# Performance work log

Hardware: AMD Instinct MI355X
Metric: run time of the kernel (lower is better)

Reference implementation:

```python
import jax, jax.numpy as jnp
import numpy as np

NUM_QUBITS = 8
QD = 2 ** NUM_QUBITS          # 256
PI = float(np.pi)
D_MODEL = 512
NUM_HEADS = 8
HEAD_DIM = D_MODEL // NUM_HEADS
LN_EPS = 1e-5


def _superposition(feat):
    # torch bug faithfully reproduced: state starts as e0 and is *multiplied*
    # by per-qubit amplitudes, so only index 0 survives. All values real.
    B, S, d = feat.shape
    idx = np.arange(NUM_QUBITS) % d
    theta = feat[:, :, idx] * PI                       # [B,S,nq]
    cos_h = jnp.cos(theta * 0.5)
    sin_h = jnp.sin(theta * 0.5)
    mask = (np.arange(QD)[None, :] >> np.arange(NUM_QUBITS)[:, None]) & 1  # [nq,QD]
    amps = jnp.where(mask[None, None] == 0, cos_h[..., None], sin_h[..., None])  # [B,S,nq,QD]
    prod = jnp.prod(amps, axis=2)                      # [B,S,QD]
    e0 = jnp.zeros((QD,), feat.dtype).at[0].set(1.0)
    state = prod * e0
    norm = jnp.sqrt(jnp.sum(state * state, axis=-1, keepdims=True))
    return state / (norm + 1e-10)


def _linear_entangle(ent):
    # entangle_matrix is block-diagonal with symmetric 2x2 blocks [[a,a],[a,-a]];
    # state @ M.T == pairwise 2x2 matmul (identical math, avoids 65536^2 matrix)
    B, S, D = ent.shape
    a = 0.7071
    M = jnp.array([[a, a], [a, -a]], ent.dtype)
    return (ent.reshape(B, S, D // 2, 2) @ M).reshape(B, S, D)


def _layer_norm(x, g, b):
    m = jnp.mean(x, axis=-1, keepdims=True)
    v = jnp.mean((x - m) ** 2, axis=-1, keepdims=True)
    return (x - m) * jax.lax.rsqrt(v + LN_EPS) * g + b


def setup_inputs() -> dict:
    key = jax.random.key(0)
    ks = jax.random.split(key, 16)
    D = D_MODEL
    s = 1.0 / np.sqrt(D)
    inp = {
        'audio_features': jax.random.normal(ks[0], (2, 256, D), jnp.float32),
        'visual_features': jax.random.normal(ks[1], (2, 256, D), jnp.float32),
        'Wq': jax.random.normal(ks[2], (D, D), jnp.float32) * s,
        'bq': jnp.zeros((D,), jnp.float32),
        'Wk': jax.random.normal(ks[3], (D, D), jnp.float32) * s,
        'bk': jnp.zeros((D,), jnp.float32),
        'Wv': jax.random.normal(ks[4], (D, D), jnp.float32) * s,
        'bv': jnp.zeros((D,), jnp.float32),
        'Wo': jax.random.normal(ks[5], (D, D), jnp.float32) * s,
        'bo': jnp.zeros((D,), jnp.float32),
        'We': jax.random.normal(ks[6], (D, D), jnp.float32) * s,
        'be': jnp.zeros((D,), jnp.float32),
        'gamma': jnp.ones((D,), jnp.float32),
        'beta': jnp.zeros((D,), jnp.float32),
    }
    return inp


def reference(audio_features, visual_features, Wq, bq, Wk, bk, Wv, bv,
              Wo, bo, We, be, gamma, beta):
    B, S, D = audio_features.shape
    H, hd = NUM_HEADS, HEAD_DIM

    aq = audio_features @ Wq + bq
    av = audio_features @ Wv + bv
    vk = visual_features @ Wk + bk
    vv = visual_features @ Wv + bv

    qa = _superposition(audio_features @ We + be)    # [B,S,QD]
    qv = _superposition(visual_features @ We + be)   # [B,S,QD]
    ent = (qa[..., :, None] * qv[..., None, :]).reshape(B, S, QD * QD)
    ent = _linear_entangle(ent)                      # [B,S,QD^2]

    probs = ent * ent
    qsum = jnp.sum(probs, axis=-1)                   # [B,S]
    ang = jnp.where(ent < 0, PI, 0.0)                # angle of a real number
    interference = jnp.cos(jnp.mean(ang, axis=-1))   # [B,S]
    scale = (qsum * interference)[:, None, :, None]  # [B,1,S,1]

    def heads(x):
        return x.reshape(B, S, H, hd).transpose(0, 2, 1, 3)

    aqh, vkh, vvh, avh = heads(aq), heads(vk), heads(vv), heads(av)
    logits = scale * jnp.einsum('bhqd,bhkd->bhqk', aqh, vkh) / np.sqrt(hd)
    attn = jax.nn.softmax(logits, axis=-1)           # [B,H,S,S]

    audio_att = jnp.einsum('bhqk,bhkd->bhqd', attn, vvh)
    visual_att = jnp.einsum('bhqk,bhqd->bhkd', attn, avh)
    audio_out = audio_att.transpose(0, 2, 1, 3).reshape(B, S, D) @ Wo + bo
    visual_out = visual_att.transpose(0, 2, 1, 3).reshape(B, S, D) @ Wo + bo

    audio_final = _layer_norm(audio_features + audio_out, gamma, beta)
    visual_final = _layer_norm(visual_features + visual_out, gamma, beta)

    quantum_coherence = jnp.mean(jnp.abs(ent))
    pn = probs / (jnp.sum(probs, axis=-1, keepdims=True) + 1e-10)
    entanglement_entropy = jnp.mean(-jnp.sum(pn * jnp.log(pn + 1e-10), axis=-1))

    return (audio_final, visual_final, quantum_coherence,
            entanglement_entropy, attn[:, -1])
```

## Files before the change

kernel.cpp:

```cpp
#include <hip/hip_runtime.h>
#include <math.h>

#define PI_F 3.14159265358979323846f

typedef __attribute__((ext_vector_type(8))) short short8v;
typedef __attribute__((ext_vector_type(4))) float f32x4;
typedef __attribute__((ext_vector_type(16))) float f32x16;

__device__ __forceinline__ unsigned short f2bf(float f) {
    unsigned int u = __float_as_uint(f);
    u += 0x7fffu + ((u >> 16) & 1u);
    return (unsigned short)(u >> 16);
}

__device__ __forceinline__ unsigned int cvtpk_bf16(float lo, float hi) {
    unsigned int r;
    asm("v_cvt_pk_bf16_f32 %0, %1, %2" : "=v"(r) : "v"(lo), "v"(hi));
    return r;
}

union W8 { unsigned int w[4]; short8v v; };

__device__ __forceinline__ void gload_lds16(const void* g, void* l) {
    __builtin_amdgcn_global_load_lds((const __attribute__((address_space(1))) unsigned int*)g,
                                     (__attribute__((address_space(3))) unsigned int*)l, 16, 0, 0);
}

__global__ __launch_bounds__(256) void prep_tok(const float* __restrict__ audio,
                                                const float* __restrict__ visual,
                                                const float* __restrict__ Wq,
                                                const float* __restrict__ Wk,
                                                const float* __restrict__ Wv,
                                                const float* __restrict__ Wo,
                                                const float* __restrict__ We,
                                                const float* __restrict__ be,
                                                unsigned short* __restrict__ audio_b,
                                                unsigned short* __restrict__ visual_b,
                                                unsigned short* __restrict__ Wqt,
                                                unsigned short* __restrict__ Wkt,
                                                unsigned short* __restrict__ Wvt,
                                                unsigned short* __restrict__ Wot,
                                                float* __restrict__ scale,
                                                float* __restrict__ coh_tok,
                                                float* __restrict__ ent_tok) {
    __shared__ float tile[32][33];
    const int bid = blockIdx.x;
    if (bid < 1536) {
        const int z = bid >> 8;
        const int x0 = (bid & 15) * 32, y0 = ((bid >> 4) & 15) * 32;
        const int tx = threadIdx.x & 31, ty = threadIdx.x >> 5;
        if (z < 2) {
            const float* src = z ? visual : audio;
            unsigned short* dst = z ? visual_b : audio_b;
#pragma unroll
            for (int i = 0; i < 4; i++) {
                int r = y0 + ty + i * 8;
                dst[r * 512 + x0 + tx] = f2bf(src[r * 512 + x0 + tx]);
            }
        } else {
            const float* src = (z == 2) ? Wq : (z == 3) ? Wk : (z == 4) ? Wv : Wo;
            unsigned short* dst = (z == 2) ? Wqt : (z == 3) ? Wkt : (z == 4) ? Wvt : Wot;
#pragma unroll
            for (int i = 0; i < 4; i++)
                tile[ty + i * 8][tx] = src[(y0 + ty + i * 8) * 512 + x0 + tx];
            __syncthreads();
#pragma unroll
            for (int i = 0; i < 4; i++) {
                int n = x0 + ty + i * 8;
                dst[n * 512 + y0 + tx] = f2bf(tile[tx][ty + i * 8]);
            }
        }
    } else {
        const int t = (bid - 1536) * 4 + (threadIdx.x >> 6);
        const int lane = threadIdx.x & 63;
        float accA[8] = {}, accV[8] = {};
#pragma unroll
        for (int i = 0; i < 8; i++) {
            int k = i * 64 + lane;
            float wa = audio[t * 512 + k], wv = visual[t * 512 + k];
            const float* wrow = &We[k * 512];
#pragma unroll
            for (int c = 0; c < 8; c++) {
                float w = wrow[c];
                accA[c] += wa * w;
                accV[c] += wv * w;
            }
        }
#pragma unroll
        for (int c = 0; c < 8; c++) {
#pragma unroll
            for (int o = 32; o >= 1; o >>= 1) {
                accA[c] += __shfl_xor(accA[c], o);
                accV[c] += __shfl_xor(accV[c], o);
            }
        }
        if (lane == 0) {
            float pa = 1.f, pv = 1.f;
#pragma unroll
            for (int c = 0; c < 8; c++) {
                pa *= cosf((accA[c] + be[c]) * (PI_F * 0.5f));
                pv *= cosf((accV[c] + be[c]) * (PI_F * 0.5f));
            }
            float s0a = pa / (fabsf(pa) + 1e-10f);
            float s0v = pv / (fabsf(pv) + 1e-10f);
            float e = s0a * s0v;
            const float a = 0.7071f;
            float ent0 = a * e;
            float qsum = 2.f * ent0 * ent0;
            float interf = (ent0 < 0.f) ? cosf(2.f * PI_F / 65536.f) : 1.f;
            scale[t] = qsum * interf;
            coh_tok[t] = 2.f * fabsf(ent0);
            float p = (ent0 * ent0) / (qsum + 1e-10f);
            ent_tok[t] = -2.f * p * logf(p + 1e-10f);
        }
    }
}

struct MfmaArgs {
    const unsigned short* A[4];
    const unsigned short* Bt[4];
    const float* bias[4];
    void* C[4];
    int obf[4];
    int otr[4];
};

__global__ __launch_bounds__(256) void gemm_mfma(MfmaArgs args) {
    const int zb = blockIdx.z;
    const unsigned short* __restrict__ A = args.A[zb];
    const unsigned short* __restrict__ Bt = args.Bt[zb];
    const float* __restrict__ bias = args.bias[zb];
    const int otr = args.otr[zb];

    const int n0 = blockIdx.x * 32;
    const int m0 = blockIdx.y * 32;

    __shared__ unsigned short As[32 * 512];
    __shared__ unsigned short Bs[32 * 512];

    const int tid = threadIdx.x;
    const int lane = tid & 63;
    const int wid = tid >> 6;
    const int wr = wid >> 1, wc = wid & 1;
    const int l15 = lane & 15;
    const int lhi = lane >> 4;

#pragma unroll
    for (int i = 0; i < 8; i++) {
        int row = i * 4 + wid;
        int lc = lane ^ row;
        gload_lds16(A + (size_t)(m0 + row) * 512 + lc * 8,
                    (char*)As + row * 1024);
        gload_lds16(Bt + (size_t)(n0 + row) * 512 + lc * 8,
                    (char*)Bs + row * 1024);
    }
    __syncthreads();

    f32x4 acc = {};
    const int arow = wr * 16 + l15;
    const int brow = wc * 16 + l15;
#pragma unroll
    for (int ks = 0; ks < 16; ks++) {
        const int lcr = ks * 4 + lhi;
        short8v a = *(const short8v*)((const char*)As + arow * 1024 + ((lcr ^ arow) << 4));
        short8v b = *(const short8v*)((const char*)Bs + brow * 1024 + ((lcr ^ brow) << 4));
        if (otr)
            acc = __builtin_amdgcn_mfma_f32_16x16x32_bf16(b, a, acc, 0, 0, 0);
        else
            acc = __builtin_amdgcn_mfma_f32_16x16x32_bf16(a, b, acc, 0, 0, 0);
    }

    if (otr) {
        unsigned short* __restrict__ Ct = (unsigned short*)args.C[zb];
#pragma unroll
        for (int r = 0; r < 4; r++) {
            int nrow = n0 + wc * 16 + lhi * 4 + r;
            int tcol = m0 + wr * 16 + l15;
            Ct[nrow * 512 + tcol] = f2bf(acc[r] + bias[nrow]);
        }
    } else if (args.obf[zb]) {
        unsigned short* __restrict__ Cb = (unsigned short*)args.C[zb];
#pragma unroll
        for (int r = 0; r < 4; r++) {
            int row = m0 + wr * 16 + lhi * 4 + r;
            int col = n0 + wc * 16 + l15;
            Cb[row * 512 + col] = f2bf(acc[r] + bias[col]);
        }
    } else {
        float* __restrict__ C = (float*)args.C[zb];
#pragma unroll
        for (int r = 0; r < 4; r++) {
            int row = m0 + wr * 16 + lhi * 4 + r;
            int col = n0 + wc * 16 + l15;
            C[row * 512 + col] = acc[r] + bias[col];
        }
    }
}

__global__ __launch_bounds__(512, 2) void attn_roles(const unsigned short* __restrict__ aqb,
                                                     const unsigned short* __restrict__ vkb,
                                                     const unsigned short* __restrict__ vvt,
                                                     const unsigned short* __restrict__ avt,
                                                     const float* __restrict__ scale,
                                                     const float* __restrict__ coh,
                                                     const float* __restrict__ entt,
                                                     unsigned short* __restrict__ attcat_b,
                                                     float* __restrict__ attn_last,
                                                     float* __restrict__ scal_out) {
    __shared__ char smem[65536];
    char* Kb = smem;
    char* VF = smem + 32768;

    const int tid = threadIdx.x;
    const int wid = tid >> 6;
    const int lane = tid & 63;
    const int lq = lane & 31;
    const int hi = lane >> 5;

    if (blockIdx.x == 8) {
        if (blockIdx.y || blockIdx.z) return;
        float c = coh[tid], e = entt[tid];
#pragma unroll
        for (int o = 32; o >= 1; o >>= 1) {
            c += __shfl_xor(c, o);
            e += __shfl_xor(e, o);
        }
        float* rc = (float*)smem;
        float* re = rc + 8;
        if (lane == 0) { rc[wid] = c; re[wid] = e; }
        __syncthreads();
        if (tid == 0) {
            float cs = 0.f, es = 0.f;
#pragma unroll
            for (int i = 0; i < 8; i++) { cs += rc[i]; es += re[i]; }
            scal_out[0] = cs / (512.f * 65536.f);
            scal_out[1] = es / 512.f;
        }
        return;
    }

    const int h = blockIdx.x, b = blockIdx.y, role = blockIdx.z;

    short8v qf[4];
    {
        const unsigned short* qbase = aqb + (size_t)(b * 256 + wid * 32 + lq) * 512 + h * 64;
#pragma unroll
        for (int s = 0; s < 4; s++) qf[s] = *(const short8v*)(qbase + (2 * s + hi) * 8);
    }
    const float sq = scale[b * 256 + wid * 32 + lq] * 0.125f;

    {
#pragma unroll
        for (int i = 0; i < 4; i++) {
            int r = wid * 32 + i * 8 + (lane >> 3);
            int lc = (lane & 7) ^ (r & 7);
            gload_lds16(vkb + (size_t)(b * 256 + r) * 512 + h * 64 + lc * 8,
                        Kb + wid * 4096 + i * 1024);
        }
    }

    {
        const unsigned short* tsrc = (role == 0) ? vvt : avt;
#pragma unroll
        for (int i = 0; i < 4; i++) {
            gload_lds16(tsrc + (size_t)(h * 64 + 32 * hi + lq) * 512 + b * 256 + 32 * wid + 8 * i,
                        VF + wid * 4096 + i * 1024);
        }
    }
    __syncthreads();

    f32x16 p[8] = {};
#pragma unroll
    for (int t = 0; t < 8; t++) {
        const int krow = t * 32 + lq;
#pragma unroll
        for (int s = 0; s < 4; s++) {
            int slot = (2 * s + hi) ^ (krow & 7);
            short8v kf = *(const short8v*)(Kb + krow * 128 + (slot << 4));
            p[t] = __builtin_amdgcn_mfma_f32_32x32x16_bf16(kf, qf[s], p[t], 0, 0, 0);
        }
    }

    {
        float mx = -1e30f;
#pragma unroll
        for (int t = 0; t < 8; t++) {
            p[t] *= sq;
#pragma unroll
            for (int r = 0; r < 16; r++) mx = fmaxf(mx, p[t][r]);
        }
        mx = fmaxf(mx, __shfl_xor(mx, 32));
        float sum = 0.f;
#pragma unroll
        for (int t = 0; t < 8; t++)
#pragma unroll
            for (int r = 0; r < 16; r++) {
                float e = __expf(p[t][r] - mx);
                p[t][r] = e;
                sum += e;
            }
        sum += __shfl_xor(sum, 32);
        float inv = 1.0f / sum;
#pragma unroll
        for (int t = 0; t < 8; t++) p[t] *= inv;
    }

    if (role == 0) {
        f32x16 aacc[2] = {};
#pragma unroll
        for (int t = 0; t < 8; t++) {
            unsigned int c0 = cvtpk_bf16(p[t][0], p[t][1]);
            unsigned int c1 = cvtpk_bf16(p[t][2], p[t][3]);
            unsigned int c2 = cvtpk_bf16(p[t][4], p[t][5]);
            unsigned int c3 = cvtpk_bf16(p[t][6], p[t][7]);
            unsigned int e0 = (unsigned int)__shfl_xor((int)c0, 32);
            unsigned int e1 = (unsigned int)__shfl_xor((int)c1, 32);
            unsigned int e2 = (unsigned int)__shfl_xor((int)c2, 32);
            unsigned int e3 = (unsigned int)__shfl_xor((int)c3, 32);
            W8 fa0;
            fa0.w[0] = hi ? e2 : c0;
            fa0.w[1] = hi ? e3 : c1;
            fa0.w[2] = hi ? c2 : e0;
            fa0.w[3] = hi ? c3 : e1;
            unsigned int c4 = cvtpk_bf16(p[t][8], p[t][9]);
            unsigned int c5 = cvtpk_bf16(p[t][10], p[t][11]);
            unsigned int c6 = cvtpk_bf16(p[t][12], p[t][13]);
            unsigned int c7 = cvtpk_bf16(p[t][14], p[t][15]);
            unsigned int e4 = (unsigned int)__shfl_xor((int)c4, 32);
            unsigned int e5 = (unsigned int)__shfl_xor((int)c5, 32);
            unsigned int e6 = (unsigned int)__shfl_xor((int)c6, 32);
            unsigned int e7 = (unsigned int)__shfl_xor((int)c7, 32);
            W8 fa1;
            fa1.w[0] = hi ? e6 : c4;
            fa1.w[1] = hi ? e7 : c5;
            fa1.w[2] = hi ? c6 : e4;
            fa1.w[3] = hi ? c7 : e5;
#pragma unroll
            for (int dt = 0; dt < 2; dt++) {
                short8v vf = *(const short8v*)(VF + ((((t * 4 + hi) * 2 + dt) * 32 + lq) << 4));
                aacc[dt] = __builtin_amdgcn_mfma_f32_32x32x16_bf16(fa0.v, vf, aacc[dt], 0, 0, 0);
                short8v vg = *(const short8v*)(VF + ((((t * 4 + hi + 2) * 2 + dt) * 32 + lq) << 4));
                aacc[dt] = __builtin_amdgcn_mfma_f32_32x32x16_bf16(fa1.v, vg, aacc[dt], 0, 0, 0);
            }
        }
#pragma unroll
        for (int dt = 0; dt < 2; dt++)
#pragma unroll
            for (int r = 0; r < 16; r++) {
                int qrow = wid * 32 + (r & 3) + 8 * (r >> 2) + 4 * hi;
                attcat_b[(size_t)(b * 256 + qrow) * 512 + h * 64 + 32 * dt + lq] = f2bf(aacc[dt][r]);
            }
        __syncthreads();

        if (h == 7) {
            float* tile = (float*)smem + (size_t)wid * (32 * 33);
            const int q2 = lane >> 1, koff = (lane & 1) * 16;
#pragma unroll
            for (int t = 0; t < 8; t++) {
#pragma unroll
                for (int r = 0; r < 16; r++)
                    tile[lq * 33 + ((r & 3) + 8 * (r >> 2) + 4 * hi)] = p[t][r];
                float* orow = attn_last + (size_t)(b * 256 + wid * 32 + q2) * 256 + 32 * t + koff;
#pragma unroll
                for (int j = 0; j < 16; j++) orow[j] = tile[q2 * 33 + koff + j];
            }
        }
        return;
    }

    __syncthreads();

    if ((wid >> 1) == 0) {
        const int dq = (wid & 1) * 32 + lq;
#pragma unroll
        for (int t = 0; t < 8; t++)
#pragma unroll
            for (int r = 0; r < 16; r++) {
                int k = 32 * t + (r & 3) + 8 * (r >> 2) + 4 * hi;
                int slot = (dq >> 3) ^ ((k ^ (k >> 3)) & 7);
                *(unsigned short*)(Kb + k * 128 + slot * 16 + (dq & 7) * 2) = f2bf(p[t][r]);
            }
    }
    __syncthreads();

    f32x16 vacc[2] = {};
    {
        const int krow = wid * 32 + lq;
        const int xr = (krow ^ (krow >> 3)) & 7;
#pragma unroll
        for (int c = 0; c < 4; c++) {
#pragma unroll
            for (int uc = 0; uc < 4; uc++) {
                int slot = (2 * uc + hi) ^ xr;
                short8v pa = *(const short8v*)(Kb + krow * 128 + slot * 16);
                int m = 2 * (4 * c + uc) + hi;
#pragma unroll
                for (int dt = 0; dt < 2; dt++) {
                    short8v af = *(const short8v*)(VF + (((m * 2 + dt) * 32 + lq) << 4));
                    vacc[dt] = __builtin_amdgcn_mfma_f32_32x32x16_bf16(pa, af, vacc[dt], 0, 0, 0);
                }
            }
            if (c < 3) {
                __syncthreads();
                if ((wid >> 1) == c + 1) {
                    const int dq = (wid & 1) * 32 + lq;
#pragma unroll
                    for (int t = 0; t < 8; t++)
#pragma unroll
                        for (int r = 0; r < 16; r++) {
                            int k = 32 * t + (r & 3) + 8 * (r >> 2) + 4 * hi;
                            int slot = (dq >> 3) ^ ((k ^ (k >> 3)) & 7);
                            *(unsigned short*)(Kb + k * 128 + slot * 16 + (dq & 7) * 2) = f2bf(p[t][r]);
                        }
                }
                __syncthreads();
            }
        }
    }
#pragma unroll
    for (int dt = 0; dt < 2; dt++)
#pragma unroll
        for (int r = 0; r < 16; r++) {
            int krow = wid * 32 + (r & 3) + 8 * (r >> 2) + 4 * hi;
            attcat_b[(size_t)(512 + b * 256 + krow) * 512 + h * 64 + 32 * dt + lq] = f2bf(vacc[dt][r]);
        }
}

__global__ __launch_bounds__(256) void ln_final(const float* __restrict__ xa,
                                                const float* __restrict__ xv,
                                                const float* __restrict__ proj,
                                                const float* __restrict__ gamma,
                                                const float* __restrict__ beta,
                                                float* __restrict__ out) {
    __shared__ float red[4];
    const int t = blockIdx.x;
    const int tid = threadIdx.x;
    const int wid = tid >> 6, lane = tid & 63;

    const float* x = (t < 512) ? (xa + t * 512) : (xv + (t - 512) * 512);
    const float* pp = proj + t * 512;

    float y0 = x[tid] + pp[tid];
    float y1 = x[tid + 256] + pp[tid + 256];

    float s = y0 + y1;
#pragma unroll
    for (int o = 32; o >= 1; o >>= 1) s += __shfl_xor(s, o);
    if (lane == 0) red[wid] = s;
    __syncthreads();
    float mean = (red[0] + red[1] + red[2] + red[3]) * (1.f / 512.f);

    float d0 = y0 - mean, d1 = y1 - mean;
    float v = d0 * d0 + d1 * d1;
    __syncthreads();
#pragma unroll
    for (int o = 32; o >= 1; o >>= 1) v += __shfl_xor(v, o);
    if (lane == 0) red[wid] = v;
    __syncthreads();
    float var = (red[0] + red[1] + red[2] + red[3]) * (1.f / 512.f);
    float rstd = rsqrtf(var + 1e-5f);

    out[t * 512 + tid] = d0 * rstd * gamma[tid] + beta[tid];
    out[t * 512 + tid + 256] = d1 * rstd * gamma[tid + 256] + beta[tid + 256];
}

extern "C" void kernel_launch(void* const* d_in, const int* in_sizes, int n_in,
                              void* d_out, int out_size, void* d_ws, size_t ws_size,
                              hipStream_t stream) {
    const float* audio  = (const float*)d_in[0];
    const float* visual = (const float*)d_in[1];
    const float* Wq = (const float*)d_in[2];
    const float* bq = (const float*)d_in[3];
    const float* Wk = (const float*)d_in[4];
    const float* bk = (const float*)d_in[5];
    const float* Wv = (const float*)d_in[6];
    const float* bv = (const float*)d_in[7];
    const float* Wo = (const float*)d_in[8];
    const float* bo = (const float*)d_in[9];
    const float* We = (const float*)d_in[10];
    const float* be = (const float*)d_in[11];
    const float* gamma = (const float*)d_in[12];
    const float* beta  = (const float*)d_in[13];
    float* out = (float*)d_out;

    float* ws = (float*)d_ws;
    float* proj  = ws;
    float* scale = ws + 524288;
    float* coh   = ws + 524800;
    float* entt  = ws + 525312;
    unsigned short* attcat_b = (unsigned short*)(ws + 525824);
    unsigned short* audio_b  = (unsigned short*)(ws + 787968);
    unsigned short* visual_b = (unsigned short*)(ws + 919040);
    unsigned short* Wqt  = (unsigned short*)(ws + 1050112);
    unsigned short* Wkt  = (unsigned short*)(ws + 1181184);
    unsigned short* Wvt  = (unsigned short*)(ws + 1312256);
    unsigned short* Wot  = (unsigned short*)(ws + 1443328);
    unsigned short* aq_b = (unsigned short*)(ws + 1574400);
    unsigned short* vk_b = (unsigned short*)(ws + 1705472);
    unsigned short* vvt  = (unsigned short*)(ws + 1836544);
    unsigned short* avt  = (unsigned short*)(ws + 1967616);

    hipLaunchKernelGGL(prep_tok, dim3(1664), dim3(256), 0, stream,
                       audio, visual, Wq, Wk, Wv, Wo, We, be,
                       audio_b, visual_b, Wqt, Wkt, Wvt, Wot,
                       scale, coh, entt);

    MfmaArgs g1;
    g1.A[0] = audio_b;  g1.Bt[0] = Wqt; g1.bias[0] = bq; g1.C[0] = aq_b; g1.obf[0] = 1; g1.otr[0] = 0;
    g1.A[1] = visual_b; g1.Bt[1] = Wkt; g1.bias[1] = bk; g1.C[1] = vk_b; g1.obf[1] = 1; g1.otr[1] = 0;
    g1.A[2] = visual_b; g1.Bt[2] = Wvt; g1.bias[2] = bv; g1.C[2] = vvt;  g1.obf[2] = 1; g1.otr[2] = 1;
    g1.A[3] = audio_b;  g1.Bt[3] = Wvt; g1.bias[3] = bv; g1.C[3] = avt;  g1.obf[3] = 1; g1.otr[3] = 1;
    hipLaunchKernelGGL(gemm_mfma, dim3(16, 16, 4), dim3(256), 0, stream, g1);

    hipLaunchKernelGGL(attn_roles, dim3(9, 2, 2), dim3(512), 0, stream,
                       aq_b, vk_b, vvt, avt, scale, coh, entt,
                       attcat_b, out + 524290, out + 524288);

    MfmaArgs g2;
    for (int i = 0; i < 4; i++) {
        g2.A[i] = attcat_b; g2.Bt[i] = Wot; g2.bias[i] = bo; g2.C[i] = proj;
        g2.obf[i] = 0; g2.otr[i] = 0;
    }
    hipLaunchKernelGGL(gemm_mfma, dim3(16, 32, 1), dim3(256), 0, stream, g2);

    hipLaunchKernelGGL(ln_final, dim3(1024), dim3(256), 0, stream,
                       audio, visual, proj, gamma, beta, out);
}
```

Before: 47.56 us.

## Fuse fp32-to-bf16 conversion and weight transpose into GEMM tile staging

Removes the separate prep kernel that converted activations to bf16 and transposed the weights into bf16 buffers. The projection GEMM and the output GEMM now read fp32 inputs and weights directly, converting and transposing them while staging tiles into shared memory, and the token-scale computation rides along in the same launch. This drops one kernel launch and the round trip through intermediate bf16 buffers. In exchange, each GEMM block redoes the conversion and does strided column loads of the weights, and each weight tile is converted many times across blocks.

```diff
diff --git a/kernel.cpp b/kernel.cpp
--- a/kernel.cpp
+++ b/kernel.cpp
@@ -26,53 +26,94 @@
                                      (__attribute__((address_space(3))) unsigned int*)l, 16, 0, 0);
 }
 
-__global__ __launch_bounds__(256) void prep_tok(const float* __restrict__ audio,
-                                                const float* __restrict__ visual,
-                                                const float* __restrict__ Wq,
-                                                const float* __restrict__ Wk,
-                                                const float* __restrict__ Wv,
-                                                const float* __restrict__ Wo,
-                                                const float* __restrict__ We,
-                                                const float* __restrict__ be,
-                                                unsigned short* __restrict__ audio_b,
-                                                unsigned short* __restrict__ visual_b,
-                                                unsigned short* __restrict__ Wqt,
-                                                unsigned short* __restrict__ Wkt,
-                                                unsigned short* __restrict__ Wvt,
-                                                unsigned short* __restrict__ Wot,
-                                                float* __restrict__ scale,
-                                                float* __restrict__ coh_tok,
-                                                float* __restrict__ ent_tok) {
-    __shared__ float tile[32][33];
+
+__device__ __forceinline__ void stageA_f32(const float* __restrict__ Af, int m0,
+                                           char* As, int tid) {
+    const int row = tid >> 3;
+    const int cb = tid & 7;
+#pragma unroll
+    for (int j = 0; j < 8; j++) {
+        int lc = cb + j * 8;
+        const float* p = Af + (size_t)(m0 + row) * 512 + lc * 8;
+        float4 a0 = *(const float4*)(p);
+        float4 a1 = *(const float4*)(p + 4);
+        W8 u;
+        u.w[0] = cvtpk_bf16(a0.x, a0.y);
+        u.w[1] = cvtpk_bf16(a0.z, a0.w);
+        u.w[2] = cvtpk_bf16(a1.x, a1.y);
+        u.w[3] = cvtpk_bf16(a1.z, a1.w);
+        *(short8v*)(As + row * 1024 + (((lc ^ row) & 63) << 4)) = u.v;
+    }
+}
+
+__device__ __forceinline__ void stageA_bf16(const unsigned short* __restrict__ Ab, int m0,
+                                            char* As, int lane, int wid) {
+#pragma unroll
+    for (int i = 0; i < 8; i++) {
+        int row = i * 4 + wid;
+        int lc = lane ^ row;
+        gload_lds16(Ab + (size_t)(m0 + row) * 512 + lc * 8, As + row * 1024);
+    }
+}
+
+__device__ __forceinline__ void stageB_tr(const float* __restrict__ W, int n0,
+                                          char* Bs, int tid) {
+    const int n = tid & 31;
+    const int kbase = (tid >> 5) * 2;
+#pragma unroll
+    for (int i = 0; i < 32; i++) {
+        int k = kbase + i * 16;
+        float lo = W[(size_t)k * 512 + n0 + n];
+        float hi = W[(size_t)(k + 1) * 512 + n0 + n];
+        unsigned int pk = cvtpk_bf16(lo, hi);
+        *(unsigned int*)(Bs + n * 1024 + (((k >> 3) ^ n) & 63) * 16 + (k & 7) * 2) = pk;
+    }
+}
+
+__device__ __forceinline__ f32x4 gemm_core(const char* As, const char* Bs,
+                                           int wr, int wc, int l15, int lhi, int otr) {
+    f32x4 acc = {};
+    const int arow = wr * 16 + l15;
+    const int brow = wc * 16 + l15;
+#pragma unroll
+    for (int ks = 0; ks < 16; ks++) {
+        const int lcr = ks * 4 + lhi;
+        short8v a = *(const short8v*)(As + arow * 1024 + ((lcr ^ arow) << 4));
+        short8v b = *(const short8v*)(Bs + brow * 1024 + ((lcr ^ brow) << 4));
+        if (otr)
+            acc = __builtin_amdgcn_mfma_f32_16x16x32_bf16(b, a, acc, 0, 0, 0);
+        else
+            acc = __builtin_amdgcn_mfma_f32_16x16x32_bf16(a, b, acc, 0, 0, 0);
+    }
+    return acc;
+}
+
+__global__ __launch_bounds__(256) void gemm1_fused(const float* __restrict__ audio,
+                                                   const float* __restrict__ visual,
+                                                   const float* __restrict__ Wq,
+                                                   const float* __restrict__ Wk,
+                                                   const float* __restrict__ Wv,
+                                                   const float* __restrict__ We,
+                                                   const float* __restrict__ be,
+                                                   const float* __restrict__ bq,
+                                                   const float* __restrict__ bk,
+                                                   const float* __restrict__ bv,
+                                                   unsigned short* __restrict__ aq_b,
+                                                   unsigned short* __restrict__ vk_b,
+                                                   unsigned short* __restrict__ vvt,
+                                                   unsigned short* __restrict__ avt,
+                                                   float* __restrict__ scale,
+                                                   float* __restrict__ coh_tok,
+                                                   float* __restrict__ ent_tok) {
+    __shared__ char As[32 * 1024];
+    __shared__ char Bs[32 * 1024];
+
     const int bid = blockIdx.x;
-    if (bid < 1536) {
-        const int z = bid >> 8;
-        const int x0 = (bid & 15) * 32, y0 = ((bid >> 4) & 15) * 32;
-        const int tx = threadIdx.x & 31, ty = threadIdx.x >> 5;
-        if (z < 2) {
-            const float* src = z ? visual : audio;
-            unsigned short* dst = z ? visual_b : audio_b;
-#pragma unroll
-            for (int i = 0; i < 4; i++) {
-                int r = y0 + ty + i * 8;
-                dst[r * 512 + x0 + tx] = f2bf(src[r * 512 + x0 + tx]);
-            }
-        } else {
-            const float* src = (z == 2) ? Wq : (z == 3) ? Wk : (z == 4) ? Wv : Wo;
-            unsigned short* dst = (z == 2) ? Wqt : (z == 3) ? Wkt : (z == 4) ? Wvt : Wot;
-#pragma unroll
-            for (int i = 0; i < 4; i++)
-                tile[ty + i * 8][tx] = src[(y0 + ty + i * 8) * 512 + x0 + tx];
-            __syncthreads();
-#pragma unroll
-            for (int i = 0; i < 4; i++) {
-                int n = x0 + ty + i * 8;
-                dst[n * 512 + y0 + tx] = f2bf(tile[tx][ty + i * 8]);
-            }
-        }
-    } else {
-        const int t = (bid - 1536) * 4 + (threadIdx.x >> 6);
-        const int lane = threadIdx.x & 63;
+    const int tid = threadIdx.x;
+
+    if (bid >= 1024) {
+        const int t = (bid - 1024) * 4 + (tid >> 6);
+        const int lane = tid & 63;
         float accA[8] = {}, accV[8] = {};
 #pragma unroll
         for (int i = 0; i < 8; i++) {
@@ -113,31 +154,59 @@
             float p = (ent0 * ent0) / (qsum + 1e-10f);
             ent_tok[t] = -2.f * p * logf(p + 1e-10f);
         }
-    }
-}
-
-struct MfmaArgs {
-    const unsigned short* A[4];
-    const unsigned short* Bt[4];
-    const float* bias[4];
-    void* C[4];
-    int obf[4];
-    int otr[4];
-};
-
-__global__ __launch_bounds__(256) void gemm_mfma(MfmaArgs args) {
-    const int zb = blockIdx.z;
-    const unsigned short* __restrict__ A = args.A[zb];
-    const unsigned short* __restrict__ Bt = args.Bt[zb];
-    const float* __restrict__ bias = args.bias[zb];
-    const int otr = args.otr[zb];
+        return;
+    }
+
+    const int z = bid >> 8;
+    const int rem = bid & 255;
+    const int n0 = (rem & 15) * 32;
+    const int m0 = (rem >> 4) * 32;
+
+    const float* A = (z == 0 || z == 3) ? audio : visual;
+    const float* W = (z == 0) ? Wq : (z == 1) ? Wk : Wv;
+    const float* bias = (z == 0) ? bq : (z == 1) ? bk : bv;
+    const int otr = (z >= 2);
+
+    stageA_f32(A, m0, As, tid);
+    stageB_tr(W, n0, Bs, tid);
+    __syncthreads();
+
+    const int lane = tid & 63;
+    const int wid = tid >> 6;
+    const int wr = wid >> 1, wc = wid & 1;
+    const int l15 = lane & 15;
+    const int lhi = lane >> 4;
+
+    f32x4 acc = gemm_core(As, Bs, wr, wc, l15, lhi, otr);
+
+    if (otr) {
+        unsigned short* Ct = (z == 2) ? vvt : avt;
+#pragma unroll
+        for (int r = 0; r < 4; r++) {
+            int nrow = n0 + wc * 16 + lhi * 4 + r;
+            int tcol = m0 + wr * 16 + l15;
+            Ct[(size_t)nrow * 512 + tcol] = f2bf(acc[r] + bias[nrow]);
+        }
+    } else {
+        unsigned short* Cb = (z == 0) ? aq_b : vk_b;
+#pragma unroll
+        for (int r = 0; r < 4; r++) {
+            int row = m0 + wr * 16 + lhi * 4 + r;
+            int col = n0 + wc * 16 + l15;
+            Cb[(size_t)row * 512 + col] = f2bf(acc[r] + bias[col]);
+        }
+    }
+}
+
+__global__ __launch_bounds__(256) void gemm2_k(const unsigned short* __restrict__ Ab,
+                                               const float* __restrict__ Wo,
+                                               const float* __restrict__ bo,
+                                               float* __restrict__ C) {
+    __shared__ char As[32 * 1024];
+    __shared__ char Bs[32 * 1024];
 
     const int n0 = blockIdx.x * 32;
     const int m0 = blockIdx.y * 32;
-
-    __shared__ unsigned short As[32 * 512];
-    __shared__ unsigned short Bs[32 * 512];
-
     const int tid = threadIdx.x;
     const int lane = tid & 63;
     const int wid = tid >> 6;
@@ -145,55 +214,17 @@
     const int l15 = lane & 15;
     const int lhi = lane >> 4;
 
-#pragma unroll
-    for (int i = 0; i < 8; i++) {
-        int row = i * 4 + wid;
-        int lc = lane ^ row;
-        gload_lds16(A + (size_t)(m0 + row) * 512 + lc * 8,
-                    (char*)As + row * 1024);
-        gload_lds16(Bt + (size_t)(n0 + row) * 512 + lc * 8,
-                    (char*)Bs + row * 1024);
-    }
-    __syncthreads();
-
-    f32x4 acc = {};
-    const int arow = wr * 16 + l15;
-    const int brow = wc * 16 + l15;
-#pragma unroll
-    for (int ks = 0; ks < 16; ks++) {
-        const int lcr = ks * 4 + lhi;
-        short8v a = *(const short8v*)((const char*)As + arow * 1024 + ((lcr ^ arow) << 4));
-        short8v b = *(const short8v*)((const char*)Bs + brow * 1024 + ((lcr ^ brow) << 4));
-        if (otr)
-            acc = __builtin_amdgcn_mfma_f32_16x16x32_bf16(b, a, acc, 0, 0, 0);
-        else
-            acc = __builtin_amdgcn_mfma_f32_16x16x32_bf16(a, b, acc, 0, 0, 0);
-    }
-
-    if (otr) {
-        unsigned short* __restrict__ Ct = (unsigned short*)args.C[zb];
-#pragma unroll
-        for (int r = 0; r < 4; r++) {
-            int nrow = n0 + wc * 16 + lhi * 4 + r;
-            int tcol = m0 + wr * 16 + l15;
-            Ct[nrow * 512 + tcol] = f2bf(acc[r] + bias[nrow]);
-        }
-    } else if (args.obf[zb]) {
-        unsigned short* __restrict__ Cb = (unsigned short*)args.C[zb];
-#pragma unroll
-        for (int r = 0; r < 4; r++) {
-            int row = m0 + wr * 16 + lhi * 4 + r;
-            int col = n0 + wc * 16 + l15;
-            Cb[row * 512 + col] = f2bf(acc[r] + bias[col]);
-        }
-    } else {
-        float* __restrict__ C = (float*)args.C[zb];
-#pragma unroll
-        for (int r = 0; r < 4; r++) {
-            int row = m0 + wr * 16 + lhi * 4 + r;
-            int col = n0 + wc * 16 + l15;
-            C[row * 512 + col] = acc[r] + bias[col];
-        }
+    stageA_bf16(Ab, m0, As, lane, wid);
+    stageB_tr(Wo, n0, Bs, tid);
+    __syncthreads();
+
+    f32x4 acc = gemm_core(As, Bs, wr, wc, l15, lhi, 0);
+
+#pragma unroll
+    for (int r = 0; r < 4; r++) {
+        int row = m0 + wr * 16 + lhi * 4 + r;
+        int col = n0 + wc * 16 + l15;
+        C[(size_t)row * 512 + col] = acc[r] + bo[col];
     }
 }
 
@@ -489,39 +520,21 @@
     float* coh   = ws + 524800;
     float* entt  = ws + 525312;
     unsigned short* attcat_b = (unsigned short*)(ws + 525824);
-    unsigned short* audio_b  = (unsigned short*)(ws + 787968);
-    unsigned short* visual_b = (unsigned short*)(ws + 919040);
-    unsigned short* Wqt  = (unsigned short*)(ws + 1050112);
-    unsigned short* Wkt  = (unsigned short*)(ws + 1181184);
-    unsigned short* Wvt  = (unsigned short*)(ws + 1312256);
-    unsigned short* Wot  = (unsigned short*)(ws + 1443328);
-    unsigned short* aq_b = (unsigned short*)(ws + 1574400);
-    unsigned short* vk_b = (unsigned short*)(ws + 1705472);
-    unsigned short* vvt  = (unsigned short*)(ws + 1836544);
-    unsigned short* avt  = (unsigned short*)(ws + 1967616);
-
-    hipLaunchKernelGGL(prep_tok, dim3(1664), dim3(256), 0, stream,
-                       audio, visual, Wq, Wk, Wv, Wo, We, be,
-                       audio_b, visual_b, Wqt, Wkt, Wvt, Wot,
-                       scale, coh, entt);
-
-    MfmaArgs g1;
-    g1.A[0] = audio_b;  g1.Bt[0] = Wqt; g1.bias[0] = bq; g1.C[0] = aq_b; g1.obf[0] = 1; g1.otr[0] = 0;
-    g1.A[1] = visual_b; g1.Bt[1] = Wkt; g1.bias[1] = bk; g1.C[1] = vk_b; g1.obf[1] = 1; g1.otr[1] = 0;
-    g1.A[2] = visual_b; g1.Bt[2] = Wvt; g1.bias[2] = bv; g1.C[2] = vvt;  g1.obf[2] = 1; g1.otr[2] = 1;
-    g1.A[3] = audio_b;  g1.Bt[3] = Wvt; g1.bias[3] = bv; g1.C[3] = avt;  g1.obf[3] = 1; g1.otr[3] = 1;
-    hipLaunchKernelGGL(gemm_mfma, dim3(16, 16, 4), dim3(256), 0, stream, g1);
+    unsigned short* aq_b = (unsigned short*)(ws + 787968);
+    unsigned short* vk_b = (unsigned short*)(ws + 919040);
+    unsigned short* vvt  = (unsigned short*)(ws + 1050112);
+    unsigned short* avt  = (unsigned short*)(ws + 1181184);
+
+    hipLaunchKernelGGL(gemm1_fused, dim3(1152), dim3(256), 0, stream,
+                       audio, visual, Wq, Wk, Wv, We, be, bq, bk, bv,
+                       aq_b, vk_b, vvt, avt, scale, coh, entt);
 
     hipLaunchKernelGGL(attn_roles, dim3(9, 2, 2), dim3(512), 0, stream,
                        aq_b, vk_b, vvt, avt, scale, coh, entt,
                        attcat_b, out + 524290, out + 524288);
 
-    MfmaArgs g2;
-    for (int i = 0; i < 4; i++) {
-        g2.A[i] = attcat_b; g2.Bt[i] = Wot; g2.bias[i] = bo; g2.C[i] = proj;
-        g2.obf[i] = 0; g2.otr[i] = 0;
-    }
-    hipLaunchKernelGGL(gemm_mfma, dim3(16, 32, 1), dim3(256), 0, stream, g2);
+    hipLaunchKernelGGL(gemm2_k, dim3(16, 32), dim3(256), 0, stream,
+                       attcat_b, Wo, bo, proj);
 
     hipLaunchKernelGGL(ln_final, dim3(1024), dim3(256), 0, stream,
                        audio, visual, proj, gamma, beta, out);
```

Result: slower. 49.12 us (+3.3%).
